# Kernel optimization log

Measured on AMD Instinct MI355X. Metric: run time of the kernel, lower is better.

The kernel has to match this reference:

```python
import jax, jax.numpy as jnp
import numpy as np

N = 6144
M_VID = 1024
M_AUD = 128
APPERTURE = 20
EPS = 1e-6


def setup_inputs() -> dict:
    key = jax.random.key(0)
    ks = jax.random.split(key, 16)
    s = 0.02
    inp = {
        "x": jax.random.normal(ks[0], (1, N, M_VID), dtype=jnp.float32),
        "x_audio": jax.random.normal(ks[1], (1, N, M_AUD), dtype=jnp.float32),
        "seq_len": N,
        "audio_len": N,
        # video self-attention (torch Linear convention: W is [out, in])
        "Wk_v": jax.random.normal(ks[2], (M_VID, M_VID), dtype=jnp.float32) * s,
        "Wq_v": jax.random.normal(ks[3], (M_VID, M_VID), dtype=jnp.float32) * s,
        "Wv_v": jax.random.normal(ks[4], (M_VID, M_VID), dtype=jnp.float32) * s,
        "Wo_v": jax.random.normal(ks[5], (M_VID, M_VID), dtype=jnp.float32) * s,
        # audio self-attention
        "Wk_a": jax.random.normal(ks[6], (M_AUD, M_AUD), dtype=jnp.float32) * s,
        "Wq_a": jax.random.normal(ks[7], (M_AUD, M_AUD), dtype=jnp.float32) * s,
        "Wv_a": jax.random.normal(ks[8], (M_AUD, M_AUD), dtype=jnp.float32) * s,
        "Wo_a": jax.random.normal(ks[9], (M_AUD, M_AUD), dtype=jnp.float32) * s,
        # MLP head
        "ka_w": jax.random.normal(ks[10], (1024, M_VID + M_AUD), dtype=jnp.float32) * s,
        "ka_b": jnp.zeros((1024,), dtype=jnp.float32),
        "kd_w": jax.random.normal(ks[11], (1, 1024), dtype=jnp.float32) * s,
        "kd_b": jnp.zeros((1,), dtype=jnp.float32),
        # layer norms
        "ln_y_g": jnp.ones((M_VID,), dtype=jnp.float32),
        "ln_y_b": jnp.zeros((M_VID,), dtype=jnp.float32),
        "ln_ya_g": jnp.ones((M_AUD,), dtype=jnp.float32),
        "ln_ya_b": jnp.zeros((M_AUD,), dtype=jnp.float32),
        "ln_ka_g": jnp.ones((1024,), dtype=jnp.float32),
        "ln_ka_b": jnp.zeros((1024,), dtype=jnp.float32),
    }
    return inp


def _layer_norm(x, g, b):
    mu = jnp.mean(x, axis=-1, keepdims=True)
    var = jnp.mean((x - mu) ** 2, axis=-1, keepdims=True)
    return (x - mu) / jnp.sqrt(var + EPS) * g + b


def _self_attention(x, Wk, Wq, Wv, Wo):
    # x: [N, d]
    n = x.shape[0]
    K = x @ Wk.T
    Q = (x @ Wq.T) * 0.06
    V = x @ Wv.T
    logits = Q @ K.T  # [N, N]
    # keep only |i-j| < apperture (trimask masks |i-j| >= apperture)
    idx = jnp.arange(n)
    band = jnp.abs(idx[:, None] - idx[None, :]) < APPERTURE
    logits = jnp.where(band, logits, -jnp.inf)
    att = jax.nn.softmax(logits, axis=-1)  # [N, N]
    # torch: y = (V^T @ att)^T == att^T @ V  (note the transpose on att!)
    y = att.T @ V
    return y @ Wo.T, att


def reference(x, x_audio, seq_len, audio_len,
              Wk_v, Wq_v, Wv_v, Wo_v,
              Wk_a, Wq_a, Wv_a, Wo_a,
              ka_w, ka_b, kd_w, kd_b,
              ln_y_g, ln_y_b, ln_ya_g, ln_ya_b, ln_ka_g, ln_ka_b):
    m = x.shape[2]
    m_audio = x_audio.shape[2]
    xf = x.reshape(-1, m)            # [N, 1024]
    xa = x_audio.reshape(-1, m_audio)  # [N, 128]

    y, att_w = _self_attention(xf, Wk_v, Wq_v, Wv_v, Wo_v)
    y = _layer_norm(y + xf, ln_y_g, ln_y_b)

    ya, att_wa = _self_attention(xa, Wk_a, Wq_a, Wv_a, Wo_a)
    ya = _layer_norm(ya + xa, ln_ya_g, ln_ya_b)

    y_comb = jnp.concatenate((y, ya), axis=1)        # [N, 1152]
    att_comb = jnp.concatenate((att_w, att_wa), axis=1)  # [N, 2N]

    h = jax.nn.relu(y_comb @ ka_w.T + ka_b)
    h = _layer_norm(h, ln_ka_g, ln_ka_b)
    score = jax.nn.sigmoid(h @ kd_w.T + kd_b)  # [N, 1]
    score = score.reshape(1, -1)               # [1, N]
    return score, att_comb
```

## Files before the change

kernel.cpp:

```cpp
#include <hip/hip_runtime.h>
#include <stdint.h>

typedef unsigned short u16;
typedef unsigned int u32;
typedef __attribute__((ext_vector_type(8))) short bf16x8;
typedef __attribute__((ext_vector_type(4))) short s16x4;
typedef __attribute__((ext_vector_type(4))) float f32x4;
typedef __attribute__((ext_vector_type(2))) float f32x2;

#define DEV __device__ __forceinline__

DEV u16 f2bf(float f) {
  union { float f; unsigned u; } v; v.f = f;
  unsigned r = v.u + 0x7fffu + ((v.u >> 16) & 1u);
  return (u16)(r >> 16);
}
DEV float bf2f(u16 h) {
  union { u32 u; float f; } v; v.u = ((u32)h) << 16; return v.f;
}
DEV float lo16(u32 w) { union { u32 u; float f; } v; v.u = w << 16; return v.f; }
DEV float hi16(u32 w) { union { u32 u; float f; } v; v.u = w & 0xFFFF0000u; return v.f; }
DEV int imax(int a, int b) { return a > b ? a : b; }
DEV int imin(int a, int b) { return a < b ? a : b; }

DEV void g2lds16(const u16* g, u16* l) {
  __builtin_amdgcn_global_load_lds(
      (const __attribute__((address_space(1))) void*)g,
      (__attribute__((address_space(3))) void*)l, 16, 0, 0);
}

#define NSEG 11
struct CastTab {
  const float* src[NSEG];
  u16* dst[NSEG];
  int start[NSEG + 1];
};

__global__ __launch_bounds__(256) void vas_cast(CastTab t, int total4) {
  int idx = blockIdx.x * 256 + threadIdx.x;
  if (idx >= total4) return;
  int s = 0;
#pragma unroll
  for (int k = 1; k < NSEG; ++k)
    if (idx >= t.start[k]) s = k;
  int local = idx - t.start[s];
  f32x4 f = ((const f32x4*)t.src[s])[local];
  s16x4 o;
  o.x = (short)f2bf(f.x);
  o.y = (short)f2bf(f.y);
  o.z = (short)f2bf(f.z);
  o.w = (short)f2bf(f.w);
  ((s16x4*)t.dst[s])[local] = o;
}

struct GemmP {
  const u16* A;
  const u16* W;
  void* C;
  const float* bias;
  int M, Nn, K, mode;
};

__global__ __launch_bounds__(256) void vas_gemm2(GemmP p0, GemmP p1, int split) {
  const bool first = blockIdx.x < (u32)split;
  GemmP p = first ? p0 : p1;
  const int bid = first ? blockIdx.x : blockIdx.x - split;

  __shared__ u16 As[2][128 * 32];
  __shared__ u16 Ws[2][128 * 32];
  const int tid = threadIdx.x;
  const int lane = tid & 63;
  const int wave = tid >> 6;

  const int Mb = p.M >> 7, Nb = p.Nn >> 7;
  const int GM = 8;
  int per = GM * Nb;
  int g = bid / per;
  int rem = bid - g * per;
  int gm = imin(GM, Mb - g * GM);
  int mblk = g * GM + rem % gm;
  int nblk = rem / gm;
  const int m0 = mblk * 128;
  const int n0 = nblk * 128;
  const int wm = (wave >> 1) * 64;
  const int wn = (wave & 1) * 64;

  const int smat = wave >> 1;
  const int skh = wave & 1;
  const u16* ssrc = smat ? p.W : p.A;
  const int sbase = smat ? n0 : m0;
  u16* sdstBase = (smat ? &Ws[skh][0] : &As[skh][0]) + lane * 8;
  const int srow = lane >> 2;
  const int scol = (lane & 3) * 8;

  f32x4 acc[4][4] = {};

  for (int k0 = 0; k0 < p.K; k0 += 64) {
#pragma unroll
    for (int u = 0; u < 8; ++u) {
      int r0 = u * 16;
      g2lds16(ssrc + (size_t)(sbase + r0 + srow) * p.K + (k0 + skh * 32 + scol),
              sdstBase + r0 * 32);
    }
    __syncthreads();
#pragma unroll
    for (int kk = 0; kk < 2; ++kk) {
      bf16x8 af[4], bfr[4];
#pragma unroll
      for (int t = 0; t < 4; ++t)
        af[t] = *(const bf16x8*)(&As[kk][0] + (wm + t * 16 + (lane & 15)) * 32 + (lane >> 4) * 8);
#pragma unroll
      for (int t = 0; t < 4; ++t)
        bfr[t] = *(const bf16x8*)(&Ws[kk][0] + (wn + t * 16 + (lane & 15)) * 32 + (lane >> 4) * 8);
#pragma unroll
      for (int mi = 0; mi < 4; ++mi)
#pragma unroll
        for (int ni = 0; ni < 4; ++ni)
          acc[mi][ni] = __builtin_amdgcn_mfma_f32_16x16x32_bf16(af[mi], bfr[ni], acc[mi][ni], 0, 0, 0);
    }
    __syncthreads();
  }

#pragma unroll
  for (int mi = 0; mi < 4; ++mi) {
#pragma unroll
    for (int ni = 0; ni < 4; ++ni) {
      int col = n0 + wn + ni * 16 + (lane & 15);
      float bv = p.bias ? p.bias[col] : 0.f;
#pragma unroll
      for (int r = 0; r < 4; ++r) {
        int row = m0 + wm + mi * 16 + (lane >> 4) * 4 + r;
        float vv = acc[mi][ni][r] + bv;
        size_t idx = (size_t)row * p.Nn + col;
        if (p.mode == 0) ((float*)p.C)[idx] = vv;
        else if (p.mode == 1) ((u16*)p.C)[idx] = f2bf(fmaxf(vv, 0.f));
        else ((u16*)p.C)[idx] = f2bf(vv);
      }
    }
  }
}

__global__ __launch_bounds__(256) void vas_battn(
    const u16* __restrict__ QKVv, const u16* __restrict__ QKVa,
    float* __restrict__ bandV, float* __restrict__ bandA,
    float* __restrict__ attBase, int N, float scale, int vb) {
  const int lane = threadIdx.x & 63;
  const int wave = threadIdx.x >> 6;
  const bool video = blockIdx.x < (u32)vb;
  const int i = (video ? blockIdx.x : blockIdx.x - vb) * 4 + wave;
  const int lo = imax(i - 19, 0);
  const int hi = imin(i + 19, N - 1);
  const int nj = hi - lo + 1;
  float logit = 0.f;
  __shared__ float a_sh[4][40];

  if (video) {
    float qf[16];
    const u16* qrow = QKVv + (size_t)i * 3072 + 1024;
#pragma unroll
    for (int c = 0; c < 2; ++c) {
      bf16x8 qv = *(const bf16x8*)(qrow + c * 512 + lane * 8);
      const u32* qw = (const u32*)&qv;
#pragma unroll
      for (int t = 0; t < 4; ++t) {
        qf[c * 8 + 2 * t] = lo16(qw[t]);
        qf[c * 8 + 2 * t + 1] = hi16(qw[t]);
      }
    }
#pragma unroll 2
    for (int s = 0; s < nj; ++s) {
      const u16* kr = QKVv + (size_t)(lo + s) * 3072;
      float p = 0.f;
#pragma unroll
      for (int c = 0; c < 2; ++c) {
        bf16x8 kv = *(const bf16x8*)(kr + c * 512 + lane * 8);
        const u32* kw = (const u32*)&kv;
#pragma unroll
        for (int t = 0; t < 4; ++t)
          p += lo16(kw[t]) * qf[c * 8 + 2 * t] + hi16(kw[t]) * qf[c * 8 + 2 * t + 1];
      }
#pragma unroll
      for (int off = 32; off; off >>= 1) p += __shfl_xor(p, off);
      if (lane == s) logit = p;
    }
  } else {
    u32 q = *(const u32*)(QKVa + (size_t)i * 384 + 128 + lane * 2);
    float q0 = lo16(q), q1 = hi16(q);
#pragma unroll 2
    for (int s = 0; s < nj; ++s) {
      u32 k = *(const u32*)(QKVa + (size_t)(lo + s) * 384 + lane * 2);
      float p = lo16(k) * q0 + hi16(k) * q1;
#pragma unroll
      for (int off = 32; off; off >>= 1) p += __shfl_xor(p, off);
      if (lane == s) logit = p;
    }
  }

  logit *= scale;
  float v = (lane < nj) ? logit : -3.4e38f;
  float mx = v;
#pragma unroll
  for (int off = 32; off; off >>= 1) mx = fmaxf(mx, __shfl_xor(mx, off));
  float e = (lane < nj) ? __expf(v - mx) : 0.f;
  float den = e;
#pragma unroll
  for (int off = 32; off; off >>= 1) den += __shfl_xor(den, off);
  float att = (lane < nj) ? e / den : 0.f;
  float* band = video ? bandV : bandA;
  if (lane < 40) {
    band[i * 40 + lane] = att;
    a_sh[wave][lane] = att;
  }

  f32x4* rowp = (f32x4*)(attBase + (size_t)i * 2 * N + (video ? 0 : N));
  const int nchunks = N / 4;
  const int cLo = lo >> 2, cHi = hi >> 2;
  for (int c = lane; c < nchunks; c += 64) {
    f32x4 o = {0.f, 0.f, 0.f, 0.f};
    if (c >= cLo && c <= cHi) {
      int col0 = c * 4;
#pragma unroll
      for (int e2 = 0; e2 < 4; ++e2) {
        int col = col0 + e2;
        if (col >= lo && col <= hi) o[e2] = a_sh[wave][col - lo];
      }
    }
    rowp[c] = o;
  }
}

#define JT 8
__global__ __launch_bounds__(256) void vas_apply(
    const u16* __restrict__ QKVv, const u16* __restrict__ QKVa,
    const float* __restrict__ bandV, const float* __restrict__ bandA,
    u16* __restrict__ Yv, u16* __restrict__ Ya, int N, int vb) {
  const int tid = threadIdx.x;
  __shared__ float a_sh[(JT + 38) * JT];

  if (blockIdx.x < (u32)vb) {
    const int j0 = blockIdx.x * JT;
    const int base = j0 - 19;
    for (int idx = tid; idx < (JT + 38) * JT; idx += 256) {
      int s = idx / JT, jj = idx % JT;
      int i = base + s;
      int j = j0 + jj;
      float w = 0.f;
      if (i >= 0 && i < N) {
        int d = j - i;
        if (d > -20 && d < 20) w = bandV[i * 40 + (j - imax(i - 19, 0))];
      }
      a_sh[s * JT + jj] = w;
    }
    __syncthreads();

    f32x4 acc[JT] = {};
    const int sLo = imax(0, -base);
    const int sHi = imin(JT + 38, N - base);
    for (int s = sLo; s < sHi; ++s) {
      s16x4 raw = *(const s16x4*)(QKVv + (size_t)(base + s) * 3072 + 2048 + tid * 4);
      f32x4 vv;
      vv.x = bf2f((u16)raw.x);
      vv.y = bf2f((u16)raw.y);
      vv.z = bf2f((u16)raw.z);
      vv.w = bf2f((u16)raw.w);
#pragma unroll
      for (int jj = 0; jj < JT; ++jj) {
        float a = a_sh[s * JT + jj];
        acc[jj].x += a * vv.x;
        acc[jj].y += a * vv.y;
        acc[jj].z += a * vv.z;
        acc[jj].w += a * vv.w;
      }
    }
#pragma unroll
    for (int jj = 0; jj < JT; ++jj) {
      s16x4 o;
      o.x = (short)f2bf(acc[jj].x);
      o.y = (short)f2bf(acc[jj].y);
      o.z = (short)f2bf(acc[jj].z);
      o.w = (short)f2bf(acc[jj].w);
      *(s16x4*)(Yv + (size_t)(j0 + jj) * 1024 + tid * 4) = o;
    }
  } else {
    const int lane = tid & 63;
    const int wave = tid >> 6;
    const int j = (blockIdx.x - vb) * 4 + wave;
    const int lo = imax(j - 19, 0);
    const int hi = imin(j + 19, N - 1);
    const int ni = hi - lo + 1;
    float* aw = a_sh + wave * 40;
    if (lane < ni) {
      int i = lo + lane;
      aw[lane] = bandA[i * 40 + (j - imax(i - 19, 0))];
    }
    __syncthreads();
    f32x2 acc = {0.f, 0.f};
#pragma unroll 4
    for (int s = 0; s < ni; ++s) {
      float a = aw[s];
      u32 k = *(const u32*)(QKVa + (size_t)(lo + s) * 384 + 256 + lane * 2);
      acc.x += a * lo16(k);
      acc.y += a * hi16(k);
    }
    u32 o = (u32)f2bf(acc.x) | ((u32)f2bf(acc.y) << 16);
    *(u32*)(Ya + (size_t)j * 128 + lane * 2) = o;
  }
}

__global__ __launch_bounds__(256) void vas_ln(
    const u16* __restrict__ Ov, const float* __restrict__ Xv,
    const float* __restrict__ gv, const float* __restrict__ bv_,
    const u16* __restrict__ Oa, const float* __restrict__ Xa,
    const float* __restrict__ ga, const float* __restrict__ ba,
    u16* __restrict__ out, int outStride, int N) {
  const int blk = blockIdx.x;
  const int tid = threadIdx.x, lane = tid & 63, wave = tid >> 6;
  __shared__ float shA[4], shB[4];

  if (blk < N) {
    const int row = blk;
    s16x4 o4 = ((const s16x4*)(Ov + (size_t)row * 1024))[tid];
    f32x4 x4 = ((const f32x4*)(Xv + (size_t)row * 1024))[tid];
    f32x4 v;
    v.x = bf2f((u16)o4.x) + x4.x;
    v.y = bf2f((u16)o4.y) + x4.y;
    v.z = bf2f((u16)o4.z) + x4.z;
    v.w = bf2f((u16)o4.w) + x4.w;
    float s = v.x + v.y + v.z + v.w;
    float s2 = v.x * v.x + v.y * v.y + v.z * v.z + v.w * v.w;
#pragma unroll
    for (int off = 32; off; off >>= 1) {
      s += __shfl_xor(s, off);
      s2 += __shfl_xor(s2, off);
    }
    if (lane == 0) { shA[wave] = s; shB[wave] = s2; }
    __syncthreads();
    float S = shA[0] + shA[1] + shA[2] + shA[3];
    float S2 = shB[0] + shB[1] + shB[2] + shB[3];
    float mu = S / 1024.f;
    float var = S2 / 1024.f - mu * mu;
    float inv = rsqrtf(var + 1e-6f);
    f32x4 gg = ((const f32x4*)gv)[tid];
    f32x4 bb = ((const f32x4*)bv_)[tid];
    s16x4 o;
    o.x = (short)f2bf((v.x - mu) * inv * gg.x + bb.x);
    o.y = (short)f2bf((v.y - mu) * inv * gg.y + bb.y);
    o.z = (short)f2bf((v.z - mu) * inv * gg.z + bb.z);
    o.w = (short)f2bf((v.w - mu) * inv * gg.w + bb.w);
    *(s16x4*)(out + (size_t)row * outStride + tid * 4) = o;
  } else {
    const int row = blk - N;
    float v = 0.f;
    if (tid < 128) v = bf2f(Oa[(size_t)row * 128 + tid]) + Xa[(size_t)row * 128 + tid];
    float s = v, s2 = v * v;
#pragma unroll
    for (int off = 32; off; off >>= 1) {
      s += __shfl_xor(s, off);
      s2 += __shfl_xor(s2, off);
    }
    if (lane == 0) { shA[wave] = s; shB[wave] = s2; }
    __syncthreads();
    float S = shA[0] + shA[1];
    float S2 = shB[0] + shB[1];
    float mu = S / 128.f;
    float var = S2 / 128.f - mu * mu;
    float inv = rsqrtf(var + 1e-6f);
    if (tid < 128)
      out[(size_t)row * outStride + 1024 + tid] =
          f2bf((v - mu) * inv * ga[tid] + ba[tid]);
  }
}

__global__ __launch_bounds__(256) void vas_head(
    const u16* __restrict__ H, const float* __restrict__ g,
    const float* __restrict__ bb, const float* __restrict__ kw,
    const float* __restrict__ kb, float* __restrict__ score) {
  const int row = blockIdx.x;
  const int tid = threadIdx.x, lane = tid & 63, wave = tid >> 6;
  __shared__ float shA[4], shB[4];
  s16x4 raw = ((const s16x4*)(H + (size_t)row * 1024))[tid];
  f32x4 v;
  v.x = bf2f((u16)raw.x);
  v.y = bf2f((u16)raw.y);
  v.z = bf2f((u16)raw.z);
  v.w = bf2f((u16)raw.w);
  float s = v.x + v.y + v.z + v.w;
  float s2 = v.x * v.x + v.y * v.y + v.z * v.z + v.w * v.w;
#pragma unroll
  for (int off = 32; off; off >>= 1) {
    s += __shfl_xor(s, off);
    s2 += __shfl_xor(s2, off);
  }
  if (lane == 0) { shA[wave] = s; shB[wave] = s2; }
  __syncthreads();
  float S = shA[0] + shA[1] + shA[2] + shA[3];
  float S2 = shB[0] + shB[1] + shB[2] + shB[3];
  float mu = S / 1024.f;
  float var = S2 / 1024.f - mu * mu;
  float inv = rsqrtf(var + 1e-6f);
  f32x4 gg = ((const f32x4*)g)[tid];
  f32x4 bv = ((const f32x4*)bb)[tid];
  f32x4 kv = ((const f32x4*)kw)[tid];
  float p = ((v.x - mu) * inv * gg.x + bv.x) * kv.x +
            ((v.y - mu) * inv * gg.y + bv.y) * kv.y +
            ((v.z - mu) * inv * gg.z + bv.z) * kv.z +
            ((v.w - mu) * inv * gg.w + bv.w) * kv.w;
#pragma unroll
  for (int off = 32; off; off >>= 1) p += __shfl_xor(p, off);
  __syncthreads();
  if (lane == 0) shA[wave] = p;
  __syncthreads();
  if (tid == 0) {
    float P = shA[0] + shA[1] + shA[2] + shA[3] + kb[0];
    score[row] = 1.f / (1.f + __expf(-P));
  }
}

extern "C" void kernel_launch(void* const* d_in, const int* in_sizes, int n_in,
                              void* d_out, int out_size, void* d_ws, size_t ws_size,
                              hipStream_t stream) {
  const float* x = (const float*)d_in[0];
  const float* xa = (const float*)d_in[1];
  const float* Wk_v = (const float*)d_in[4];
  const float* Wq_v = (const float*)d_in[5];
  const float* Wv_v = (const float*)d_in[6];
  const float* Wo_v = (const float*)d_in[7];
  const float* Wk_a = (const float*)d_in[8];
  const float* Wq_a = (const float*)d_in[9];
  const float* Wv_a = (const float*)d_in[10];
  const float* Wo_a = (const float*)d_in[11];
  const float* ka_w = (const float*)d_in[12];
  const float* ka_b = (const float*)d_in[13];
  const float* kd_w = (const float*)d_in[14];
  const float* kd_b = (const float*)d_in[15];
  const float* ln_y_g = (const float*)d_in[16];
  const float* ln_y_b = (const float*)d_in[17];
  const float* ln_ya_g = (const float*)d_in[18];
  const float* ln_ya_b = (const float*)d_in[19];
  const float* ln_ka_g = (const float*)d_in[20];
  const float* ln_ka_b = (const float*)d_in[21];

  const int N = in_sizes[0] / 1024;
  const int MV = 1024, MA = 128, MH = 1152;

  char* wsb = (char*)d_ws;
  size_t off = 0;
  auto alloc = [&](size_t bytes) -> void* {
    void* p = wsb + off;
    off += (bytes + 255) & ~(size_t)255;
    return p;
  };
  u16* xf_b    = (u16*)alloc((size_t)N * MV * 2);
  u16* xa_b    = (u16*)alloc((size_t)N * MA * 2);
  u16* wqkv_b  = (u16*)alloc((size_t)3 * MV * MV * 2);
  u16* wqkva_b = (u16*)alloc((size_t)3 * MA * MA * 2);
  u16* wov_b   = (u16*)alloc((size_t)MV * MV * 2);
  u16* woa_b   = (u16*)alloc((size_t)MA * MA * 2);
  u16* kaw_b   = (u16*)alloc((size_t)1024 * MH * 2);
  u16* QKVv    = (u16*)alloc((size_t)N * 3 * MV * 2);
  u16* QKVa    = (u16*)alloc((size_t)N * 3 * MA * 2);
  float* bandV = (float*)alloc((size_t)N * 40 * 4);
  float* bandA = (float*)alloc((size_t)N * 40 * 4);
  u16* yv_b = (u16*)alloc((size_t)N * MV * 2);
  u16* ya_b = (u16*)alloc((size_t)N * MA * 2);
  u16* ov_b = (u16*)alloc((size_t)N * MV * 2);
  u16* oa_b = (u16*)alloc((size_t)N * MA * 2);
  u16* ycomb_b = (u16*)alloc((size_t)N * MH * 2);
  u16* h_b = (u16*)alloc((size_t)N * 1024 * 2);

  float* dout = (float*)d_out;
  float* attBase = dout + N;

  {
    CastTab t;
    int c = 0, cum = 0;
    auto seg = [&](const float* s, u16* d, size_t n) {
      t.src[c] = s; t.dst[c] = d; t.start[c] = cum; cum += (int)(n / 4); ++c;
    };
    seg(x, xf_b, (size_t)N * MV);
    seg(xa, xa_b, (size_t)N * MA);
    seg(Wk_v, wqkv_b + 0 * MV * MV, (size_t)MV * MV);
    seg(Wq_v, wqkv_b + 1 * MV * MV, (size_t)MV * MV);
    seg(Wv_v, wqkv_b + 2 * MV * MV, (size_t)MV * MV);
    seg(Wk_a, wqkva_b + 0 * MA * MA, (size_t)MA * MA);
    seg(Wq_a, wqkva_b + 1 * MA * MA, (size_t)MA * MA);
    seg(Wv_a, wqkva_b + 2 * MA * MA, (size_t)MA * MA);
    seg(Wo_v, wov_b, (size_t)MV * MV);
    seg(Wo_a, woa_b, (size_t)MA * MA);
    seg(ka_w, kaw_b, (size_t)1024 * MH);
    t.start[c] = cum;
    vas_cast<<<(cum + 255) / 256, 256, 0, stream>>>(t, cum);
  }

  {
    GemmP pv = {xf_b, wqkv_b, QKVv, nullptr, N, 3 * MV, MV, 2};
    GemmP pa = {xa_b, wqkva_b, QKVa, nullptr, N, 3 * MA, MA, 2};
    int bv = (N / 128) * (3 * MV / 128);
    int ba = (N / 128) * (3 * MA / 128);
    vas_gemm2<<<bv + ba, 256, 0, stream>>>(pv, pa, bv);
  }

  vas_battn<<<N / 2, 256, 0, stream>>>(QKVv, QKVa, bandV, bandA, attBase, N, 0.06f, N / 4);

  vas_apply<<<N / JT + N / 4, 256, 0, stream>>>(QKVv, QKVa, bandV, bandA, yv_b, ya_b, N, N / JT);

  {
    GemmP pv = {yv_b, wov_b, ov_b, nullptr, N, MV, MV, 2};
    GemmP pa = {ya_b, woa_b, oa_b, nullptr, N, MA, MA, 2};
    int bv = (N / 128) * (MV / 128);
    int ba = (N / 128) * (MA / 128);
    vas_gemm2<<<bv + ba, 256, 0, stream>>>(pv, pa, bv);
  }

  vas_ln<<<2 * N, 256, 0, stream>>>(ov_b, x, ln_y_g, ln_y_b,
                                    oa_b, xa, ln_ya_g, ln_ya_b,
                                    ycomb_b, MH, N);

  {
    GemmP ph = {ycomb_b, kaw_b, h_b, ka_b, N, 1024, MH, 1};
    int bh = (N / 128) * (1024 / 128);
    vas_gemm2<<<bh, 256, 0, stream>>>(ph, ph, bh);
  }

  vas_head<<<N, 256, 0, stream>>>(h_b, ln_ka_g, ln_ka_b, kd_w, kd_b, dout);
}
```

Measured before the change: 592.6 us.

## Fold output projection into value weights and fuse band apply with layernorm

Precomputes Wo·Wv as a single weight by transposing Wv and running a small GEMM, so the value projection directly produces Wo-projected values. This removes the separate N×1024 output-projection GEMM and its intermediate buffers. The attention-apply kernel now adds the residual and applies layernorm in place, which eliminates the standalone LN kernel. It also adds XCD-aware block remapping in the GEMM and a one-step prefetch in the apply loop. The price is an extra transpose and a weight-product GEMM per call, plus a further bf16 rounding of the fused weight.

```diff
diff --git a/kernel.cpp b/kernel.cpp
--- a/kernel.cpp
+++ b/kernel.cpp
@@ -29,7 +29,7 @@
       (__attribute__((address_space(3))) void*)l, 16, 0, 0);
 }
 
-#define NSEG 11
+#define NSEG 9
 struct CastTab {
   const float* src[NSEG];
   u16* dst[NSEG];
@@ -53,6 +53,26 @@
   ((s16x4*)t.dst[s])[local] = o;
 }
 
+__global__ __launch_bounds__(256) void vas_transpose(
+    const float* __restrict__ Vv, u16* __restrict__ Tv,
+    const float* __restrict__ Va, u16* __restrict__ Ta, int nvb) {
+  __shared__ float t[32][33];
+  int b = blockIdx.x;
+  const float* src; u16* dst; int n;
+  if (b < nvb) { src = Vv; dst = Tv; n = 1024; }
+  else { b -= nvb; src = Va; dst = Ta; n = 128; }
+  const int tpr = n >> 5;
+  const int tr = (b / tpr) * 32, tc = (b % tpr) * 32;
+  const int lx = threadIdx.x & 31, ly = threadIdx.x >> 5;
+#pragma unroll
+  for (int r = 0; r < 4; ++r)
+    t[ly + r * 8][lx] = src[(size_t)(tr + ly + r * 8) * n + tc + lx];
+  __syncthreads();
+#pragma unroll
+  for (int r = 0; r < 4; ++r)
+    dst[(size_t)(tc + ly + r * 8) * n + tr + lx] = f2bf(t[lx][ly + r * 8]);
+}
+
 struct GemmP {
   const u16* A;
   const u16* W;
@@ -62,9 +82,14 @@
 };
 
 __global__ __launch_bounds__(256) void vas_gemm2(GemmP p0, GemmP p1, int split) {
-  const bool first = blockIdx.x < (u32)split;
+  const int nwg = gridDim.x;
+  const int b0 = blockIdx.x;
+  const int qq = nwg >> 3, rr = nwg & 7, xcd = b0 & 7, li = b0 >> 3;
+  const int bs = (xcd < rr ? xcd * (qq + 1) : rr * (qq + 1) + (xcd - rr) * qq) + li;
+
+  const bool first = bs < split;
   GemmP p = first ? p0 : p1;
-  const int bid = first ? blockIdx.x : blockIdx.x - split;
+  const int bid = first ? bs : bs - split;
 
   __shared__ u16 As[2][128 * 32];
   __shared__ u16 Ws[2][128 * 32];
@@ -230,12 +255,16 @@
 }
 
 #define JT 8
-__global__ __launch_bounds__(256) void vas_apply(
+__global__ __launch_bounds__(256) void vas_apply_ln(
     const u16* __restrict__ QKVv, const u16* __restrict__ QKVa,
     const float* __restrict__ bandV, const float* __restrict__ bandA,
-    u16* __restrict__ Yv, u16* __restrict__ Ya, int N, int vb) {
+    const float* __restrict__ Xv, const float* __restrict__ Xa,
+    const float* __restrict__ gv, const float* __restrict__ bv_,
+    const float* __restrict__ ga, const float* __restrict__ ba,
+    u16* __restrict__ out, int outStride, int N, int vb) {
   const int tid = threadIdx.x;
   __shared__ float a_sh[(JT + 38) * JT];
+  __shared__ float red[2][JT][4];
 
   if (blockIdx.x < (u32)vb) {
     const int j0 = blockIdx.x * JT;
@@ -256,8 +285,11 @@
     f32x4 acc[JT] = {};
     const int sLo = imax(0, -base);
     const int sHi = imin(JT + 38, N - base);
+    s16x4 nxt = *(const s16x4*)(QKVv + (size_t)(base + sLo) * 3072 + 2048 + tid * 4);
     for (int s = sLo; s < sHi; ++s) {
-      s16x4 raw = *(const s16x4*)(QKVv + (size_t)(base + s) * 3072 + 2048 + tid * 4);
+      s16x4 raw = nxt;
+      if (s + 1 < sHi)
+        nxt = *(const s16x4*)(QKVv + (size_t)(base + s + 1) * 3072 + 2048 + tid * 4);
       f32x4 vv;
       vv.x = bf2f((u16)raw.x);
       vv.y = bf2f((u16)raw.y);
@@ -272,14 +304,43 @@
         acc[jj].w += a * vv.w;
       }
     }
+
+    const int lane = tid & 63, wave = tid >> 6;
 #pragma unroll
     for (int jj = 0; jj < JT; ++jj) {
+      f32x4 x4 = ((const f32x4*)(Xv + (size_t)(j0 + jj) * 1024))[tid];
+      f32x4 v;
+      v.x = acc[jj].x + x4.x;
+      v.y = acc[jj].y + x4.y;
+      v.z = acc[jj].z + x4.z;
+      v.w = acc[jj].w + x4.w;
+      acc[jj] = v;
+      float s = v.x + v.y + v.z + v.w;
+      float s2 = v.x * v.x + v.y * v.y + v.z * v.z + v.w * v.w;
+#pragma unroll
+      for (int off = 32; off; off >>= 1) {
+        s += __shfl_xor(s, off);
+        s2 += __shfl_xor(s2, off);
+      }
+      if (lane == 0) { red[0][jj][wave] = s; red[1][jj][wave] = s2; }
+    }
+    __syncthreads();
+    f32x4 gg = ((const f32x4*)gv)[tid];
+    f32x4 bb = ((const f32x4*)bv_)[tid];
+#pragma unroll
+    for (int jj = 0; jj < JT; ++jj) {
+      float S = red[0][jj][0] + red[0][jj][1] + red[0][jj][2] + red[0][jj][3];
+      float S2 = red[1][jj][0] + red[1][jj][1] + red[1][jj][2] + red[1][jj][3];
+      float mu = S / 1024.f;
+      float var = S2 / 1024.f - mu * mu;
+      float inv = rsqrtf(var + 1e-6f);
+      f32x4 v = acc[jj];
       s16x4 o;
-      o.x = (short)f2bf(acc[jj].x);
-      o.y = (short)f2bf(acc[jj].y);
-      o.z = (short)f2bf(acc[jj].z);
-      o.w = (short)f2bf(acc[jj].w);
-      *(s16x4*)(Yv + (size_t)(j0 + jj) * 1024 + tid * 4) = o;
+      o.x = (short)f2bf((v.x - mu) * inv * gg.x + bb.x);
+      o.y = (short)f2bf((v.y - mu) * inv * gg.y + bb.y);
+      o.z = (short)f2bf((v.z - mu) * inv * gg.z + bb.z);
+      o.w = (short)f2bf((v.w - mu) * inv * gg.w + bb.w);
+      *(s16x4*)(out + (size_t)(j0 + jj) * outStride + tid * 4) = o;
     }
   } else {
     const int lane = tid & 63;
@@ -302,72 +363,23 @@
       acc.x += a * lo16(k);
       acc.y += a * hi16(k);
     }
-    u32 o = (u32)f2bf(acc.x) | ((u32)f2bf(acc.y) << 16);
-    *(u32*)(Ya + (size_t)j * 128 + lane * 2) = o;
-  }
-}
-
-__global__ __launch_bounds__(256) void vas_ln(
-    const u16* __restrict__ Ov, const float* __restrict__ Xv,
-    const float* __restrict__ gv, const float* __restrict__ bv_,
-    const u16* __restrict__ Oa, const float* __restrict__ Xa,
-    const float* __restrict__ ga, const float* __restrict__ ba,
-    u16* __restrict__ out, int outStride, int N) {
-  const int blk = blockIdx.x;
-  const int tid = threadIdx.x, lane = tid & 63, wave = tid >> 6;
-  __shared__ float shA[4], shB[4];
-
-  if (blk < N) {
-    const int row = blk;
-    s16x4 o4 = ((const s16x4*)(Ov + (size_t)row * 1024))[tid];
-    f32x4 x4 = ((const f32x4*)(Xv + (size_t)row * 1024))[tid];
-    f32x4 v;
-    v.x = bf2f((u16)o4.x) + x4.x;
-    v.y = bf2f((u16)o4.y) + x4.y;
-    v.z = bf2f((u16)o4.z) + x4.z;
-    v.w = bf2f((u16)o4.w) + x4.w;
-    float s = v.x + v.y + v.z + v.w;
-    float s2 = v.x * v.x + v.y * v.y + v.z * v.z + v.w * v.w;
+    f32x2 x2 = *(const f32x2*)(Xa + (size_t)j * 128 + lane * 2);
+    float vx = acc.x + x2.x;
+    float vy = acc.y + x2.y;
+    float s = vx + vy, s2 = vx * vx + vy * vy;
 #pragma unroll
     for (int off = 32; off; off >>= 1) {
       s += __shfl_xor(s, off);
       s2 += __shfl_xor(s2, off);
     }
-    if (lane == 0) { shA[wave] = s; shB[wave] = s2; }
-    __syncthreads();
-    float S = shA[0] + shA[1] + shA[2] + shA[3];
-    float S2 = shB[0] + shB[1] + shB[2] + shB[3];
-    float mu = S / 1024.f;
-    float var = S2 / 1024.f - mu * mu;
+    float mu = s / 128.f;
+    float var = s2 / 128.f - mu * mu;
     float inv = rsqrtf(var + 1e-6f);
-    f32x4 gg = ((const f32x4*)gv)[tid];
-    f32x4 bb = ((const f32x4*)bv_)[tid];
-    s16x4 o;
-    o.x = (short)f2bf((v.x - mu) * inv * gg.x + bb.x);
-    o.y = (short)f2bf((v.y - mu) * inv * gg.y + bb.y);
-    o.z = (short)f2bf((v.z - mu) * inv * gg.z + bb.z);
-    o.w = (short)f2bf((v.w - mu) * inv * gg.w + bb.w);
-    *(s16x4*)(out + (size_t)row * outStride + tid * 4) = o;
-  } else {
-    const int row = blk - N;
-    float v = 0.f;
-    if (tid < 128) v = bf2f(Oa[(size_t)row * 128 + tid]) + Xa[(size_t)row * 128 + tid];
-    float s = v, s2 = v * v;
-#pragma unroll
-    for (int off = 32; off; off >>= 1) {
-      s += __shfl_xor(s, off);
-      s2 += __shfl_xor(s2, off);
-    }
-    if (lane == 0) { shA[wave] = s; shB[wave] = s2; }
-    __syncthreads();
-    float S = shA[0] + shA[1];
-    float S2 = shB[0] + shB[1];
-    float mu = S / 128.f;
-    float var = S2 / 128.f - mu * mu;
-    float inv = rsqrtf(var + 1e-6f);
-    if (tid < 128)
-      out[(size_t)row * outStride + 1024 + tid] =
-          f2bf((v - mu) * inv * ga[tid] + ba[tid]);
+    f32x2 g2 = *(const f32x2*)(ga + lane * 2);
+    f32x2 b2 = *(const f32x2*)(ba + lane * 2);
+    u32 o = (u32)f2bf((vx - mu) * inv * g2.x + b2.x) |
+            ((u32)f2bf((vy - mu) * inv * g2.y + b2.y) << 16);
+    *(u32*)(out + (size_t)j * outStride + 1024 + lane * 2) = o;
   }
 }
 
@@ -456,15 +468,13 @@
   u16* wqkva_b = (u16*)alloc((size_t)3 * MA * MA * 2);
   u16* wov_b   = (u16*)alloc((size_t)MV * MV * 2);
   u16* woa_b   = (u16*)alloc((size_t)MA * MA * 2);
+  u16* wvT_b   = (u16*)alloc((size_t)MV * MV * 2);
+  u16* wvaT_b  = (u16*)alloc((size_t)MA * MA * 2);
   u16* kaw_b   = (u16*)alloc((size_t)1024 * MH * 2);
   u16* QKVv    = (u16*)alloc((size_t)N * 3 * MV * 2);
   u16* QKVa    = (u16*)alloc((size_t)N * 3 * MA * 2);
   float* bandV = (float*)alloc((size_t)N * 40 * 4);
   float* bandA = (float*)alloc((size_t)N * 40 * 4);
-  u16* yv_b = (u16*)alloc((size_t)N * MV * 2);
-  u16* ya_b = (u16*)alloc((size_t)N * MA * 2);
-  u16* ov_b = (u16*)alloc((size_t)N * MV * 2);
-  u16* oa_b = (u16*)alloc((size_t)N * MA * 2);
   u16* ycomb_b = (u16*)alloc((size_t)N * MH * 2);
   u16* h_b = (u16*)alloc((size_t)N * 1024 * 2);
 
@@ -481,15 +491,26 @@
     seg(xa, xa_b, (size_t)N * MA);
     seg(Wk_v, wqkv_b + 0 * MV * MV, (size_t)MV * MV);
     seg(Wq_v, wqkv_b + 1 * MV * MV, (size_t)MV * MV);
-    seg(Wv_v, wqkv_b + 2 * MV * MV, (size_t)MV * MV);
     seg(Wk_a, wqkva_b + 0 * MA * MA, (size_t)MA * MA);
     seg(Wq_a, wqkva_b + 1 * MA * MA, (size_t)MA * MA);
-    seg(Wv_a, wqkva_b + 2 * MA * MA, (size_t)MA * MA);
     seg(Wo_v, wov_b, (size_t)MV * MV);
     seg(Wo_a, woa_b, (size_t)MA * MA);
     seg(ka_w, kaw_b, (size_t)1024 * MH);
     t.start[c] = cum;
     vas_cast<<<(cum + 255) / 256, 256, 0, stream>>>(t, cum);
+  }
+
+  {
+    int nvb = (MV / 32) * (MV / 32);
+    int nab = (MA / 32) * (MA / 32);
+    vas_transpose<<<nvb + nab, 256, 0, stream>>>(Wv_v, wvT_b, Wv_a, wvaT_b, nvb);
+  }
+
+  {
+    GemmP pv = {wov_b, wvT_b, wqkv_b + 2 * MV * MV, nullptr, MV, MV, MV, 2};
+    GemmP pa = {woa_b, wvaT_b, wqkva_b + 2 * MA * MA, nullptr, MA, MA, MA, 2};
+    int bv = (MV / 128) * (MV / 128);
+    vas_gemm2<<<bv + 1, 256, 0, stream>>>(pv, pa, bv);
   }
 
   {
@@ -502,19 +523,9 @@
 
   vas_battn<<<N / 2, 256, 0, stream>>>(QKVv, QKVa, bandV, bandA, attBase, N, 0.06f, N / 4);
 
-  vas_apply<<<N / JT + N / 4, 256, 0, stream>>>(QKVv, QKVa, bandV, bandA, yv_b, ya_b, N, N / JT);
-
-  {
-    GemmP pv = {yv_b, wov_b, ov_b, nullptr, N, MV, MV, 2};
-    GemmP pa = {ya_b, woa_b, oa_b, nullptr, N, MA, MA, 2};
-    int bv = (N / 128) * (MV / 128);
-    int ba = (N / 128) * (MA / 128);
-    vas_gemm2<<<bv + ba, 256, 0, stream>>>(pv, pa, bv);
-  }
-
-  vas_ln<<<2 * N, 256, 0, stream>>>(ov_b, x, ln_y_g, ln_y_b,
-                                    oa_b, xa, ln_ya_g, ln_ya_b,
-                                    ycomb_b, MH, N);
+  vas_apply_ln<<<N / JT + N / 4, 256, 0, stream>>>(
+      QKVv, QKVa, bandV, bandA, x, xa,
+      ln_y_g, ln_y_b, ln_ya_g, ln_ya_b, ycomb_b, MH, N, N / JT);
 
   {
     GemmP ph = {ycomb_b, kaw_b, h_b, ka_b, N, 1024, MH, 1};
```

After: 588.8 us. No clear change (-0.6%).
